# Performance work log

Measured on AMD Instinct MI355X. Metric: run time of the kernel, lower is better.

Reference implementation:

```python
import jax, jax.numpy as jnp
import numpy as np

B, D, V, S = 8192, 128, 1000000, 8192


def setup_inputs() -> dict:
    key = jax.random.key(0)
    k1, k2, k3, k4, k5 = jax.random.split(key, 5)
    inputs = jax.random.normal(k1, (B, D), dtype=jnp.float32)
    weights = jax.random.normal(k2, (V, D), dtype=jnp.float32) * 0.05  # NCE class embeddings
    biases = jax.random.normal(k3, (V,), dtype=jnp.float32) * 0.01
    true_ids = jax.random.randint(k4, (B,), 0, V, dtype=jnp.int64)
    sampled_ids = jax.random.randint(k5, (S,), 0, V, dtype=jnp.int64)
    return {"inputs": inputs, "weights": weights, "biases": biases,
            "true_ids": true_ids, "sampled_ids": sampled_ids}


def reference(inputs, weights, biases, true_ids, sampled_ids):
    # --- sparse gathers (irregular access) ---
    w_true = weights[true_ids]          # [B, D]
    b_true = biases[true_ids]           # [B]
    w_samp = weights[sampled_ids]       # [S, D]
    b_samp = biases[sampled_ids]        # [S]

    # --- logits ---
    # true logits: per-example dot product
    logits_true = jnp.einsum('bd,bd->b', inputs, w_true) + b_true        # [B]
    # sampled logits: dense matmul against the gathered negative rows
    logits_samp = jnp.einsum('bd,sd->bs', inputs, w_samp) + b_samp[None]  # [B, S]

    # --- sigmoid cross-entropy (labels: 1 for true class, 0 for sampled) ---
    # label=1 -> softplus(-x); label=0 -> softplus(x)  (numerically stable)
    ce_true = jax.nn.softplus(-logits_true)             # [B]
    ce_samp = jnp.sum(jax.nn.softplus(logits_samp), axis=1)  # [B]

    # NCE per-example loss
    return ce_true + ce_samp  # [B]
```

## Files before the change

### kernel.cpp

```cpp
#include <hip/hip_runtime.h>
#include <cstdint>

typedef unsigned int u32;
typedef _Float16 f16;
typedef _Float16 f16x4 __attribute__((ext_vector_type(4)));
typedef _Float16 f16x8 __attribute__((ext_vector_type(8)));
typedef float f32x4 __attribute__((ext_vector_type(4)));

#define DDIM 128

typedef __attribute__((address_space(1))) u32 gu32;
typedef __attribute__((address_space(3))) u32 lu32;

__device__ __forceinline__ void direct16(const void* g, void* l) {
    __builtin_amdgcn_global_load_lds((gu32*)(uintptr_t)g, (lu32*)(uintptr_t)l, 16, 0, 0);
}

__device__ __forceinline__ float softplus_f(float x) {
    float ax = fabsf(x);
    float e  = __expf(-ax);
    return fmaxf(x, 0.0f) + __logf(1.0f + e);
}

__global__ __launch_bounds__(256) void convx_kernel(const float* __restrict__ X, f16* __restrict__ Xb) {
    int t = blockIdx.x * 256 + threadIdx.x;
    float4 v = ((const float4*)X)[t];
    f16x4 h;
    h[0] = (f16)v.x; h[1] = (f16)v.y; h[2] = (f16)v.z; h[3] = (f16)v.w;
    ((f16x4*)Xb)[t] = h;
}

__global__ __launch_bounds__(256) void gather_kernel(const float* __restrict__ W, const float* __restrict__ bias,
                                                     const int* __restrict__ sids,
                                                     f16* __restrict__ Wb, float* __restrict__ bs) {
    int t = blockIdx.x * 256 + threadIdx.x;
    int s = t >> 5, j = t & 31;
    int row = sids[s];
    float4 v = ((const float4*)(W + (size_t)row * DDIM))[j];
    f16x4 h;
    h[0] = (f16)v.x; h[1] = (f16)v.y; h[2] = (f16)v.z; h[3] = (f16)v.w;
    ((f16x4*)(Wb + (size_t)s * DDIM))[j] = h;
    if (j == 0) bs[s] = bias[row];
}

__global__ __launch_bounds__(256) void ce_true_kernel(const float* __restrict__ X, const float* __restrict__ W,
                                                      const float* __restrict__ bias, const int* __restrict__ tids,
                                                      float* __restrict__ out) {
    int gt = blockIdx.x * 256 + threadIdx.x;
    int b = gt >> 6;
    int lane = gt & 63;
    int row = tids[b];
    float2 xv = ((const float2*)(X + (size_t)b   * DDIM))[lane];
    float2 wv = ((const float2*)(W + (size_t)row * DDIM))[lane];
    float d = fmaf(xv.x, wv.x, xv.y * wv.y);
#pragma unroll
    for (int off = 32; off > 0; off >>= 1) d += __shfl_xor(d, off);
    if (lane == 0) {
        float logit = d + bias[row];
        out[b] = softplus_f(-logit);
    }
}

__global__ __launch_bounds__(256, 2) void nce_gemm(const f16* __restrict__ Xb, const f16* __restrict__ Wb,
                                                   const float* __restrict__ bs, float* __restrict__ out) {
    __shared__ __attribute__((aligned(16))) f16 As[128 * DDIM];
    __shared__ __attribute__((aligned(16))) f16 Bs[128 * DDIM];

    const int tid = threadIdx.x;
    const int bn = blockIdx.x, bm = blockIdx.y;

    {
        const char* Ag = (const char*)(Xb + (size_t)bm * 128 * DDIM);
        const char* Bg = (const char*)(Wb + (size_t)bn * 128 * DDIM);
        int t4 = tid >> 4, t0 = tid & 15;
        int src0 = t4 * 256 + ((t0 ^ t4) << 4);
        int dst0 = tid << 4;
#pragma unroll
        for (int i = 0; i < 8; ++i) {
            direct16(Ag + i * 4096 + src0, (char*)As + i * 4096 + dst0);
            direct16(Bg + i * 4096 + src0, (char*)Bs + i * 4096 + dst0);
        }
    }
    __syncthreads();

    const int lane = tid & 63;
    const int w  = tid >> 6;
    const int wm = w >> 1, wn = w & 1;
    const int l0 = lane & 15;
    const int q  = lane >> 4;

    f32x4 acc[4][4];
#pragma unroll
    for (int mi = 0; mi < 4; ++mi)
#pragma unroll
        for (int ni = 0; ni < 4; ++ni)
            acc[mi][ni] = (f32x4){0.f, 0.f, 0.f, 0.f};

#pragma unroll
    for (int ks = 0; ks < 4; ++ks) {
        f16x8 a_f[4], b_f[4];
        int g = ks * 4 + q;
#pragma unroll
        for (int mi = 0; mi < 4; ++mi) {
            int m_l = wm * 64 + mi * 16 + l0;
            a_f[mi] = *(const f16x8*)(As + m_l * DDIM + ((g ^ l0) << 3));
        }
#pragma unroll
        for (int ni = 0; ni < 4; ++ni) {
            int n_l = wn * 64 + ni * 16 + l0;
            b_f[ni] = *(const f16x8*)(Bs + n_l * DDIM + ((g ^ l0) << 3));
        }
#pragma unroll
        for (int mi = 0; mi < 4; ++mi)
#pragma unroll
            for (int ni = 0; ni < 4; ++ni)
                acc[mi][ni] = __builtin_amdgcn_mfma_f32_16x16x32_f16(a_f[mi], b_f[ni], acc[mi][ni], 0, 0, 0);
    }

    float bias_v[4];
#pragma unroll
    for (int ni = 0; ni < 4; ++ni)
        bias_v[ni] = bs[bn * 128 + wn * 64 + ni * 16 + l0];

#pragma unroll
    for (int mi = 0; mi < 4; ++mi) {
        float s0 = 0.f, s1 = 0.f, s2 = 0.f, s3 = 0.f;
#pragma unroll
        for (int ni = 0; ni < 4; ++ni) {
            f32x4 c = acc[mi][ni];
            float bv = bias_v[ni];
            s0 += softplus_f(c[0] + bv);
            s1 += softplus_f(c[1] + bv);
            s2 += softplus_f(c[2] + bv);
            s3 += softplus_f(c[3] + bv);
        }
#pragma unroll
        for (int off = 1; off < 16; off <<= 1) {
            s0 += __shfl_xor(s0, off);
            s1 += __shfl_xor(s1, off);
            s2 += __shfl_xor(s2, off);
            s3 += __shfl_xor(s3, off);
        }
        if (l0 == 0) {
            int m_g = bm * 128 + wm * 64 + mi * 16 + q * 4;
            atomicAdd(&out[m_g + 0], s0);
            atomicAdd(&out[m_g + 1], s1);
            atomicAdd(&out[m_g + 2], s2);
            atomicAdd(&out[m_g + 3], s3);
        }
    }
}

extern "C" void kernel_launch(void* const* d_in, const int* in_sizes, int n_in,
                              void* d_out, int out_size, void* d_ws, size_t ws_size,
                              hipStream_t stream) {
    const float* X  = (const float*)d_in[0];
    const float* W  = (const float*)d_in[1];
    const float* Bv = (const float*)d_in[2];
    const int*   Ti = (const int*)d_in[3];
    const int*   Si = (const int*)d_in[4];
    float* out = (float*)d_out;

    f16*   Xb = (f16*)d_ws;
    f16*   Wb = (f16*)((char*)d_ws + (2u << 20));
    float* bs = (float*)((char*)d_ws + (4u << 20));

    convx_kernel <<<1024, 256, 0, stream>>>(X, Xb);
    gather_kernel<<<1024, 256, 0, stream>>>(W, Bv, Si, Wb, bs);
    ce_true_kernel<<<2048, 256, 0, stream>>>(X, W, Bv, Ti, out);
    nce_gemm<<<dim3(64, 64), 256, 0, stream>>>(Xb, Wb, bs, out);
}
```

Baseline: 650.0 us.

## Fuse prep kernels, reshape warp tiling, use exp2/log2 softplus, replace atomics with partial reduce

Merges the X conversion and W gather into one launch. Changes the GEMM warp layout from 2x2 to 4x1, so each warp covers 32 rows and all 128 columns and the per-row reduction happens inside one warp. Computes softplus in base-2 using hardware exp2/log intrinsics with LOG2E/LN2 scaling. Replaces per-row atomicAdds with per-column-block partial sums written to workspace, then sums them in a separate reduce kernel. This removes atomic contention but adds a 2MB partial buffer and an extra small launch with only 8 blocks.

Result: faster. 593.7 us (-8.7%).

```diff
diff --git a/kernel.cpp b/kernel.cpp
--- a/kernel.cpp
+++ b/kernel.cpp
@@ -8,6 +8,9 @@
 typedef float f32x4 __attribute__((ext_vector_type(4)));
 
 #define DDIM 128
+#define NBN 64
+#define LOG2E 1.4426950408889634f
+#define LN2   0.6931471805599453f
 
 typedef __attribute__((address_space(1))) u32 gu32;
 typedef __attribute__((address_space(3))) u32 lu32;
@@ -16,31 +19,32 @@
     __builtin_amdgcn_global_load_lds((gu32*)(uintptr_t)g, (lu32*)(uintptr_t)l, 16, 0, 0);
 }
 
-__device__ __forceinline__ float softplus_f(float x) {
+__device__ __forceinline__ float softplus_exact(float x) {
     float ax = fabsf(x);
     float e  = __expf(-ax);
     return fmaxf(x, 0.0f) + __logf(1.0f + e);
 }
 
-__global__ __launch_bounds__(256) void convx_kernel(const float* __restrict__ X, f16* __restrict__ Xb) {
-    int t = blockIdx.x * 256 + threadIdx.x;
-    float4 v = ((const float4*)X)[t];
-    f16x4 h;
-    h[0] = (f16)v.x; h[1] = (f16)v.y; h[2] = (f16)v.z; h[3] = (f16)v.w;
-    ((f16x4*)Xb)[t] = h;
-}
-
-__global__ __launch_bounds__(256) void gather_kernel(const float* __restrict__ W, const float* __restrict__ bias,
-                                                     const int* __restrict__ sids,
-                                                     f16* __restrict__ Wb, float* __restrict__ bs) {
-    int t = blockIdx.x * 256 + threadIdx.x;
-    int s = t >> 5, j = t & 31;
-    int row = sids[s];
-    float4 v = ((const float4*)(W + (size_t)row * DDIM))[j];
-    f16x4 h;
-    h[0] = (f16)v.x; h[1] = (f16)v.y; h[2] = (f16)v.z; h[3] = (f16)v.w;
-    ((f16x4*)(Wb + (size_t)s * DDIM))[j] = h;
-    if (j == 0) bs[s] = bias[row];
+__global__ __launch_bounds__(256) void prep_kernel(const float* __restrict__ X, f16* __restrict__ Xb,
+                                                   const float* __restrict__ W, const float* __restrict__ bias,
+                                                   const int* __restrict__ sids,
+                                                   f16* __restrict__ Wb, float* __restrict__ bs) {
+    if (blockIdx.x < 1024) {
+        int t = blockIdx.x * 256 + threadIdx.x;
+        float4 v = ((const float4*)X)[t];
+        f16x4 h;
+        h[0] = (f16)v.x; h[1] = (f16)v.y; h[2] = (f16)v.z; h[3] = (f16)v.w;
+        ((f16x4*)Xb)[t] = h;
+    } else {
+        int t = (blockIdx.x - 1024) * 256 + threadIdx.x;
+        int s = t >> 5, j = t & 31;
+        int row = sids[s];
+        float4 v = ((const float4*)(W + (size_t)row * DDIM))[j];
+        f16x4 h;
+        h[0] = (f16)v.x; h[1] = (f16)v.y; h[2] = (f16)v.z; h[3] = (f16)v.w;
+        ((f16x4*)(Wb + (size_t)s * DDIM))[j] = h;
+        if (j == 0) bs[s] = bias[row];
+    }
 }
 
 __global__ __launch_bounds__(256) void ce_true_kernel(const float* __restrict__ X, const float* __restrict__ W,
@@ -57,12 +61,12 @@
     for (int off = 32; off > 0; off >>= 1) d += __shfl_xor(d, off);
     if (lane == 0) {
         float logit = d + bias[row];
-        out[b] = softplus_f(-logit);
+        out[b] = softplus_exact(-logit);
     }
 }
 
 __global__ __launch_bounds__(256, 2) void nce_gemm(const f16* __restrict__ Xb, const f16* __restrict__ Wb,
-                                                   const float* __restrict__ bs, float* __restrict__ out) {
+                                                   const float* __restrict__ bs, float* __restrict__ partial) {
     __shared__ __attribute__((aligned(16))) f16 As[128 * DDIM];
     __shared__ __attribute__((aligned(16))) f16 Bs[128 * DDIM];
 
@@ -85,54 +89,57 @@
 
     const int lane = tid & 63;
     const int w  = tid >> 6;
-    const int wm = w >> 1, wn = w & 1;
     const int l0 = lane & 15;
     const int q  = lane >> 4;
 
-    f32x4 acc[4][4];
+    f32x4 acc[2][8];
 #pragma unroll
-    for (int mi = 0; mi < 4; ++mi)
+    for (int mi = 0; mi < 2; ++mi)
 #pragma unroll
-        for (int ni = 0; ni < 4; ++ni)
+        for (int ni = 0; ni < 8; ++ni)
             acc[mi][ni] = (f32x4){0.f, 0.f, 0.f, 0.f};
 
 #pragma unroll
     for (int ks = 0; ks < 4; ++ks) {
-        f16x8 a_f[4], b_f[4];
+        f16x8 a_f[2], b_f[8];
         int g = ks * 4 + q;
 #pragma unroll
-        for (int mi = 0; mi < 4; ++mi) {
-            int m_l = wm * 64 + mi * 16 + l0;
+        for (int mi = 0; mi < 2; ++mi) {
+            int m_l = w * 32 + mi * 16 + l0;
             a_f[mi] = *(const f16x8*)(As + m_l * DDIM + ((g ^ l0) << 3));
         }
 #pragma unroll
-        for (int ni = 0; ni < 4; ++ni) {
-            int n_l = wn * 64 + ni * 16 + l0;
+        for (int ni = 0; ni < 8; ++ni) {
+            int n_l = ni * 16 + l0;
             b_f[ni] = *(const f16x8*)(Bs + n_l * DDIM + ((g ^ l0) << 3));
         }
 #pragma unroll
-        for (int mi = 0; mi < 4; ++mi)
+        for (int mi = 0; mi < 2; ++mi)
 #pragma unroll
-            for (int ni = 0; ni < 4; ++ni)
+            for (int ni = 0; ni < 8; ++ni)
                 acc[mi][ni] = __builtin_amdgcn_mfma_f32_16x16x32_f16(a_f[mi], b_f[ni], acc[mi][ni], 0, 0, 0);
     }
 
-    float bias_v[4];
+    float bt[8];
 #pragma unroll
-    for (int ni = 0; ni < 4; ++ni)
-        bias_v[ni] = bs[bn * 128 + wn * 64 + ni * 16 + l0];
+    for (int ni = 0; ni < 8; ++ni)
+        bt[ni] = bs[bn * 128 + ni * 16 + l0] * LOG2E;
 
 #pragma unroll
-    for (int mi = 0; mi < 4; ++mi) {
+    for (int mi = 0; mi < 2; ++mi) {
         float s0 = 0.f, s1 = 0.f, s2 = 0.f, s3 = 0.f;
 #pragma unroll
-        for (int ni = 0; ni < 4; ++ni) {
+        for (int ni = 0; ni < 8; ++ni) {
             f32x4 c = acc[mi][ni];
-            float bv = bias_v[ni];
-            s0 += softplus_f(c[0] + bv);
-            s1 += softplus_f(c[1] + bv);
-            s2 += softplus_f(c[2] + bv);
-            s3 += softplus_f(c[3] + bv);
+            float bv = bt[ni];
+            float t0 = fmaf(c[0], LOG2E, bv);
+            float t1 = fmaf(c[1], LOG2E, bv);
+            float t2 = fmaf(c[2], LOG2E, bv);
+            float t3 = fmaf(c[3], LOG2E, bv);
+            s0 += fmaxf(t0, 0.f) + __builtin_amdgcn_logf(1.f + __builtin_amdgcn_exp2f(-fabsf(t0)));
+            s1 += fmaxf(t1, 0.f) + __builtin_amdgcn_logf(1.f + __builtin_amdgcn_exp2f(-fabsf(t1)));
+            s2 += fmaxf(t2, 0.f) + __builtin_amdgcn_logf(1.f + __builtin_amdgcn_exp2f(-fabsf(t2)));
+            s3 += fmaxf(t3, 0.f) + __builtin_amdgcn_logf(1.f + __builtin_amdgcn_exp2f(-fabsf(t3)));
         }
 #pragma unroll
         for (int off = 1; off < 16; off <<= 1) {
@@ -142,13 +149,22 @@
             s3 += __shfl_xor(s3, off);
         }
         if (l0 == 0) {
-            int m_g = bm * 128 + wm * 64 + mi * 16 + q * 4;
-            atomicAdd(&out[m_g + 0], s0);
-            atomicAdd(&out[m_g + 1], s1);
-            atomicAdd(&out[m_g + 2], s2);
-            atomicAdd(&out[m_g + 3], s3);
+            int m = bm * 128 + w * 32 + mi * 16 + q * 4;
+            float4 v = make_float4(s0 * LN2, s1 * LN2, s2 * LN2, s3 * LN2);
+            *(float4*)(partial + (size_t)bn * 8192 + m) = v;
         }
     }
+}
+
+__global__ __launch_bounds__(256) void reduce_kernel(const float* __restrict__ partial, float* __restrict__ out) {
+    int t = blockIdx.x * 256 + threadIdx.x;
+    float4 s = ((const float4*)out)[t];
+#pragma unroll
+    for (int bn = 0; bn < NBN; ++bn) {
+        float4 p = ((const float4*)(partial + (size_t)bn * 8192))[t];
+        s.x += p.x; s.y += p.y; s.z += p.z; s.w += p.w;
+    }
+    ((float4*)out)[t] = s;
 }
 
 extern "C" void kernel_launch(void* const* d_in, const int* in_sizes, int n_in,
@@ -164,9 +180,10 @@
     f16*   Xb = (f16*)d_ws;
     f16*   Wb = (f16*)((char*)d_ws + (2u << 20));
     float* bs = (float*)((char*)d_ws + (4u << 20));
+    float* pp = (float*)((char*)d_ws + (5u << 20));
 
-    convx_kernel <<<1024, 256, 0, stream>>>(X, Xb);
-    gather_kernel<<<1024, 256, 0, stream>>>(W, Bv, Si, Wb, bs);
+    prep_kernel   <<<2048, 256, 0, stream>>>(X, Xb, W, Bv, Si, Wb, bs);
     ce_true_kernel<<<2048, 256, 0, stream>>>(X, W, Bv, Ti, out);
-    nce_gemm<<<dim3(64, 64), 256, 0, stream>>>(Xb, Wb, bs, out);
+    nce_gemm      <<<dim3(64, 64), 256, 0, stream>>>(Xb, Wb, bs, pp);
+    reduce_kernel <<<8, 256, 0, stream>>>(pp, out);
 }
```
